# Performance work log

Measured on AMD Instinct MI355X. Metric: run time of the kernel, lower is better.

The kernel has to match this reference:

```python
import jax, jax.numpy as jnp
import numpy as np

L, T, D, H, NC = 4, 2, 128, 8, 7
DH = D // H
DFF = 4 * D
EPS = 1e-5


def _ln(x, w, b):
    m = jnp.mean(x, axis=-1, keepdims=True)
    v = jnp.mean((x - m) ** 2, axis=-1, keepdims=True)
    return (x - m) / jnp.sqrt(v + EPS) * w + b


def setup_inputs() -> dict:
    key = jax.random.key(0)
    ks = jax.random.split(key, 16)
    s = 0.02
    inp = {
        "x": jax.random.normal(ks[0], (65536, 1, 2 * D), dtype=jnp.float32),
        "token_proj_w": jax.random.normal(ks[1], (T * D, T * D), dtype=jnp.float32) * s,
        "token_proj_b": jnp.zeros((T * D,), jnp.float32),
        "pos_emb": jax.random.normal(ks[2], (1, T, D), dtype=jnp.float32),
        "qkv_w": jax.random.normal(ks[3], (L, 3 * D, D), dtype=jnp.float32) * s,
        "qkv_b": jnp.zeros((L, 3 * D), jnp.float32),
        "out_w": jax.random.normal(ks[4], (L, D, D), dtype=jnp.float32) * s,
        "out_b": jnp.zeros((L, D), jnp.float32),
        "ln1_w": jnp.ones((L, D), jnp.float32),
        "ln1_b": jnp.zeros((L, D), jnp.float32),
        "ff1_w": jax.random.normal(ks[5], (L, DFF, D), dtype=jnp.float32) * s,
        "ff1_b": jnp.zeros((L, DFF), jnp.float32),
        "ff2_w": jax.random.normal(ks[6], (L, D, DFF), dtype=jnp.float32) * s,
        "ff2_b": jnp.zeros((L, D), jnp.float32),
        "ln2_w": jnp.ones((L, D), jnp.float32),
        "ln2_b": jnp.zeros((L, D), jnp.float32),
        "lnf_w": jnp.ones((D,), jnp.float32),
        "lnf_b": jnp.zeros((D,), jnp.float32),
        "cls_ln_w": jnp.ones((D,), jnp.float32),
        "cls_ln_b": jnp.zeros((D,), jnp.float32),
        "cls_w": jax.random.normal(ks[7], (NC, D), dtype=jnp.float32) * s,
        "cls_b": jnp.zeros((NC,), jnp.float32),
    }
    return inp


def _forward(x, token_proj_w, token_proj_b, pos_emb, qkv_w, qkv_b, out_w, out_b,
             ln1_w, ln1_b, ff1_w, ff1_b, ff2_w, ff2_b, ln2_w, ln2_b,
             lnf_w, lnf_b, cls_ln_w, cls_ln_b, cls_w, cls_b):
    x = jnp.squeeze(x, 1)                                  # [B, 256]
    B = x.shape[0]
    tok = x @ token_proj_w.T + token_proj_b                # [B, 256]
    tok = tok.reshape(B, T, D) + pos_emb                   # [B, 2, 128]
    scale = 1.0 / jnp.sqrt(jnp.float32(DH))
    for i in range(L):
        # --- self-attention (post-norm, as in nn.TransformerEncoderLayer) ---
        qkv = jnp.einsum('btd,ed->bte', tok, qkv_w[i]) + qkv_b[i]   # [B,T,3D]
        q, k, v = jnp.split(qkv, 3, axis=-1)
        q = q.reshape(B, T, H, DH)
        k = k.reshape(B, T, H, DH)
        v = v.reshape(B, T, H, DH)
        scores = jnp.einsum('bqhd,bkhd->bhqk', q, k) * scale
        attn = jax.nn.softmax(scores, axis=-1)
        o = jnp.einsum('bhqk,bkhd->bqhd', attn, v).reshape(B, T, D)
        o = jnp.einsum('btd,ed->bte', o, out_w[i]) + out_b[i]
        tok = _ln(tok + o, ln1_w[i], ln1_b[i])
        # --- FFN ---
        h = jnp.einsum('btd,fd->btf', tok, ff1_w[i]) + ff1_b[i]
        h = jax.nn.gelu(h, approximate=False)
        h = jnp.einsum('btf,df->btd', h, ff2_w[i]) + ff2_b[i]
        tok = _ln(tok + h, ln2_w[i], ln2_b[i])
    tok = _ln(tok, lnf_w, lnf_b)                           # final encoder norm
    pooled = jnp.mean(tok, axis=1)                         # [B, D]
    out = _ln(pooled, cls_ln_w, cls_ln_b)
    out = jax.nn.gelu(out, approximate=False)
    return out @ cls_w.T + cls_b                           # [B, 7]


def reference(x, token_proj_w, token_proj_b, pos_emb, qkv_w, qkv_b, out_w, out_b,
              ln1_w, ln1_b, ff1_w, ff1_b, ff2_w, ff2_b, ln2_w, ln2_b,
              lnf_w, lnf_b, cls_ln_w, cls_ln_b, cls_w, cls_b):
    return _forward(x, token_proj_w, token_proj_b, pos_emb, qkv_w, qkv_b, out_w, out_b,
                    ln1_w, ln1_b, ff1_w, ff1_b, ff2_w, ff2_b, ln2_w, ln2_b,
                    lnf_w, lnf_b, cls_ln_w, cls_ln_b, cls_w, cls_b)
```

## Files before the change

### kernel.cpp

```cpp
#include <hip/hip_runtime.h>


#define DEV static __device__ __forceinline__

typedef __attribute__((ext_vector_type(8))) short short8;
typedef __attribute__((ext_vector_type(4))) float f32x4;

#define BS    32
#define MROWS 64
#define PITCH 136
#define LEPS  1e-5f

#define OFF_TPW  0
#define OFF_QKVW 65536
#define OFF_OUTW 262144
#define OFF_FF1W 327680
#define OFF_FF2W 589824
#define WS_ELEMS 851968

DEV unsigned short f2b(float f) {
  unsigned u = __float_as_uint(f);
  return (unsigned short)((u + 0x7fffu + ((u >> 16) & 1u)) >> 16);
}
DEV float b2f(unsigned short s) { return __uint_as_float((unsigned)s << 16); }

DEV f32x4 MFMA(short8 a, short8 b, f32x4 c) {
  return __builtin_amdgcn_mfma_f32_16x16x32_bf16(a, b, c, 0, 0, 0);
}

DEV float gelu_f(float x) {
  float u = 0.7978845608028654f * (x + 0.044715f * x * x * x);
  float e = __expf(2.0f * u);
  float t = 1.0f - 2.0f / (e + 1.0f);
  return 0.5f * x * (1.0f + t);
}

DEV short8 ldfrag(const unsigned short* tile, int rowBase, int kk, int lane) {
  return *(const short8*)(tile + (rowBase + (lane & 15)) * PITCH + kk * 32 + (lane >> 4) * 8);
}

DEV void stage_f32(unsigned short* dst, const float* __restrict__ src,
                   int srcPitch, int rows, int tid) {
  int total = rows * 8;
  for (int idx = tid; idx < total; idx += 256) {
    int r = idx >> 3, s = idx & 7;
    const float4* p = (const float4*)(src + (size_t)r * srcPitch + s * 16);
    float4 f0 = p[0], f1 = p[1], f2 = p[2], f3 = p[3];
    short8 lo, hi;
    lo[0] = (short)f2b(f0.x); lo[1] = (short)f2b(f0.y);
    lo[2] = (short)f2b(f0.z); lo[3] = (short)f2b(f0.w);
    lo[4] = (short)f2b(f1.x); lo[5] = (short)f2b(f1.y);
    lo[6] = (short)f2b(f1.z); lo[7] = (short)f2b(f1.w);
    hi[0] = (short)f2b(f2.x); hi[1] = (short)f2b(f2.y);
    hi[2] = (short)f2b(f2.z); hi[3] = (short)f2b(f2.w);
    hi[4] = (short)f2b(f3.x); hi[5] = (short)f2b(f3.y);
    hi[6] = (short)f2b(f3.z); hi[7] = (short)f2b(f3.w);
    *(short8*)(dst + r * PITCH + s * 16)     = lo;
    *(short8*)(dst + r * PITCH + s * 16 + 8) = hi;
  }
}

DEV void stage_w64(unsigned short* dst, const unsigned short* __restrict__ src,
                   int srcPitch, int tid) {
  for (int idx = tid; idx < 512; idx += 256) {
    int r = idx >> 3, s = idx & 7;
    const uint4* p = (const uint4*)(src + (size_t)r * srcPitch + s * 16);
    uint4 a = p[0], b = p[1];
    *(uint4*)(dst + r * PITCH + s * 16)     = a;
    *(uint4*)(dst + r * PITCH + s * 16 + 8) = b;
  }
}

DEV void ln_residual_write(f32x4 (&val)[2][4], const float* __restrict__ w,
                           const float* __restrict__ b, unsigned short* sTok,
                           float* sRedP, float* sRedF, int tid) {
  const int wave = tid >> 6, lane = tid & 63, g = lane >> 4, j = lane & 15;
  float ps[4][4], pq[4][4];
#pragma unroll
  for (int rt = 0; rt < 4; ++rt)
#pragma unroll
    for (int r = 0; r < 4; ++r) {
      float v0 = val[0][rt][r], v1 = val[1][rt][r];
      float s = v0 + v1, q = v0 * v0 + v1 * v1;
#pragma unroll
      for (int m = 1; m < 16; m <<= 1) {
        s += __shfl_xor(s, m, 16);
        q += __shfl_xor(q, m, 16);
      }
      ps[rt][r] = s; pq[rt][r] = q;
    }
  if (j == 0) {
#pragma unroll
    for (int rt = 0; rt < 4; ++rt)
#pragma unroll
      for (int r = 0; r < 4; ++r) {
        int row = rt * 16 + g * 4 + r;
        sRedP[row * 8 + wave * 2]     = ps[rt][r];
        sRedP[row * 8 + wave * 2 + 1] = pq[rt][r];
      }
  }
  __syncthreads();
  if (tid < 64) {
    float s = 0.f, q = 0.f;
#pragma unroll
    for (int wv = 0; wv < 4; ++wv) {
      s += sRedP[tid * 8 + wv * 2];
      q += sRedP[tid * 8 + wv * 2 + 1];
    }
    float mean = s * (1.f / 128.f);
    sRedF[tid * 2]     = mean;
    sRedF[tid * 2 + 1] = rsqrtf(q * (1.f / 128.f) - mean * mean + LEPS);
  }
  __syncthreads();
#pragma unroll
  for (int h = 0; h < 2; ++h) {
    int n = (h * 4 + wave) * 16 + j;
    float wn = w[n], bn = b[n];
#pragma unroll
    for (int rt = 0; rt < 4; ++rt)
#pragma unroll
      for (int r = 0; r < 4; ++r) {
        int row = rt * 16 + g * 4 + r;
        float mean = sRedF[row * 2], rstd = sRedF[row * 2 + 1];
        sTok[row * PITCH + n] = f2b((val[h][rt][r] - mean) * rstd * wn + bn);
      }
  }
  __syncthreads();
}

__global__ __launch_bounds__(256)
void prep_w(const float* __restrict__ tpw, const float* __restrict__ qkvw,
            const float* __restrict__ outw, const float* __restrict__ ff1w,
            const float* __restrict__ ff2w, unsigned short* __restrict__ wsb) {
  int i = blockIdx.x * 256 + threadIdx.x;
  if (i >= WS_ELEMS) return;
  float v;
  if (i < OFF_QKVW)      v = tpw[i - OFF_TPW];
  else if (i < OFF_OUTW) v = qkvw[i - OFF_QKVW];
  else if (i < OFF_FF1W) v = outw[i - OFF_OUTW];
  else if (i < OFF_FF2W) v = ff1w[i - OFF_FF1W];
  else                   v = ff2w[i - OFF_FF2W];
  wsb[i] = f2b(v);
}

#define STAGE_W(srcexpr, pitch)                         \
  do {                                                  \
    __syncthreads();                                    \
    stage_w64(sB, (srcexpr), (pitch), tid);             \
    __syncthreads();                                    \
  } while (0)

__global__ __launch_bounds__(256, 2)
void tx_fused(const float* __restrict__ x, const unsigned short* __restrict__ wsb,
              const float* __restrict__ tpb, const float* __restrict__ pos,
              const float* __restrict__ qkvb, const float* __restrict__ outb,
              const float* __restrict__ ln1w, const float* __restrict__ ln1b,
              const float* __restrict__ ff1b, const float* __restrict__ ff2b,
              const float* __restrict__ ln2w, const float* __restrict__ ln2b,
              const float* __restrict__ lnfw, const float* __restrict__ lnfb,
              const float* __restrict__ clnw, const float* __restrict__ clnb,
              const float* __restrict__ cw, const float* __restrict__ cb,
              float* __restrict__ out) {
  __shared__ unsigned short sTok[MROWS * PITCH];
  __shared__ unsigned short sStage[MROWS * PITCH];
  __shared__ unsigned short sB[64 * PITCH];
  __shared__ float sRedP[MROWS * 8];
  __shared__ float sRedF[MROWS * 2];

  const int tid  = threadIdx.x;
  const int wave = tid >> 6;
  const int lane = tid & 63;
  const int g = lane >> 4, j = lane & 15;
  const size_t s0 = (size_t)blockIdx.x * BS;

  const unsigned short* tpwB  = wsb + OFF_TPW;
  const unsigned short* qkvwB = wsb + OFF_QKVW;
  const unsigned short* outwB = wsb + OFF_OUTW;
  const unsigned short* ff1wB = wsb + OFF_FF1W;
  const unsigned short* ff2wB = wsb + OFF_FF2W;

  const f32x4 zero4 = {0.f, 0.f, 0.f, 0.f};

  f32x4 accTP[2][2][2];
#pragma unroll
  for (int nc = 0; nc < 2; ++nc)
#pragma unroll
    for (int h = 0; h < 2; ++h)
#pragma unroll
      for (int rt = 0; rt < 2; ++rt) accTP[nc][h][rt] = zero4;

  for (int kc = 0; kc < 2; ++kc) {
    __syncthreads();
    stage_f32(sStage, x + s0 * 256 + kc * 128, 256, BS, tid);
    for (int nc = 0; nc < 2; ++nc)
      for (int h = 0; h < 2; ++h) {
        STAGE_W(tpwB + (size_t)(nc * 128 + h * 64) * 256 + kc * 128, 256);
        short8 bf[4];
#pragma unroll
        for (int kk = 0; kk < 4; ++kk) bf[kk] = ldfrag(sB, wave * 16, kk, lane);
#pragma unroll
        for (int rt = 0; rt < 2; ++rt)
#pragma unroll
          for (int kk = 0; kk < 4; ++kk)
            accTP[nc][h][rt] = MFMA(ldfrag(sStage, rt * 16, kk, lane), bf[kk], accTP[nc][h][rt]);
      }
  }
  __syncthreads();
#pragma unroll
  for (int nc = 0; nc < 2; ++nc)
#pragma unroll
    for (int h = 0; h < 2; ++h) {
      int d = (h * 4 + wave) * 16 + j;
      float bias = tpb[nc * 128 + d] + pos[nc * 128 + d];
#pragma unroll
      for (int rt = 0; rt < 2; ++rt)
#pragma unroll
        for (int r = 0; r < 4; ++r) {
          int sm = rt * 16 + g * 4 + r;
          sTok[(2 * sm + nc) * PITCH + d] = f2b(accTP[nc][h][rt][r] + bias);
        }
    }
  __syncthreads();

  for (int li = 0; li < 4; ++li) {
    short8 aT[4][4];
#pragma unroll
    for (int rt = 0; rt < 4; ++rt)
#pragma unroll
      for (int kk = 0; kk < 4; ++kk) aT[rt][kk] = ldfrag(sTok, rt * 16, kk, lane);

    f32x4 acc[6][4];
#pragma unroll
    for (int a = 0; a < 6; ++a)
#pragma unroll
      for (int rt = 0; rt < 4; ++rt) acc[a][rt] = zero4;

    for (int nc = 0; nc < 3; ++nc)
      for (int h = 0; h < 2; ++h) {
        STAGE_W(qkvwB + (size_t)li * 49152 + (size_t)(nc * 128 + h * 64) * 128, 128);
        short8 bf[4];
#pragma unroll
        for (int kk = 0; kk < 4; ++kk) bf[kk] = ldfrag(sB, wave * 16, kk, lane);
        int a = nc * 2 + h;
#pragma unroll
        for (int rt = 0; rt < 4; ++rt)
#pragma unroll
          for (int kk = 0; kk < 4; ++kk)
            acc[a][rt] = MFMA(aT[rt][kk], bf[kk], acc[a][rt]);
      }
#pragma unroll
    for (int a = 0; a < 6; ++a) {
      int nc = a >> 1, h = a & 1;
      float bv = qkvb[li * 384 + nc * 128 + (h * 4 + wave) * 16 + j];
#pragma unroll
      for (int rt = 0; rt < 4; ++rt) acc[a][rt] += bv;
    }

#pragma unroll
    for (int hh = 0; hh < 2; ++hh) {
      int head = hh * 4 + wave;
#pragma unroll
      for (int rt = 0; rt < 4; ++rt)
#pragma unroll
        for (int sp = 0; sp < 2; ++sp) {
          int r0 = sp * 2, r1 = r0 + 1;
          float q0 = acc[hh][rt][r0],     q1 = acc[hh][rt][r1];
          float k0 = acc[2 + hh][rt][r0], k1 = acc[2 + hh][rt][r1];
          float s00 = q0 * k0, s01 = q0 * k1, s10 = q1 * k0, s11 = q1 * k1;
#pragma unroll
          for (int m = 1; m < 16; m <<= 1) {
            s00 += __shfl_xor(s00, m, 16);
            s01 += __shfl_xor(s01, m, 16);
            s10 += __shfl_xor(s10, m, 16);
            s11 += __shfl_xor(s11, m, 16);
          }
          s00 *= 0.25f; s01 *= 0.25f; s10 *= 0.25f; s11 *= 0.25f;
          float m0 = fmaxf(s00, s01), m1 = fmaxf(s10, s11);
          float e00 = __expf(s00 - m0), e01 = __expf(s01 - m0);
          float e10 = __expf(s10 - m1), e11 = __expf(s11 - m1);
          float i0 = 1.f / (e00 + e01), i1 = 1.f / (e10 + e11);
          float v0 = acc[4 + hh][rt][r0], v1 = acc[4 + hh][rt][r1];
          float o0 = (e00 * v0 + e01 * v1) * i0;
          float o1 = (e10 * v0 + e11 * v1) * i1;
          int rowb = rt * 16 + g * 4 + r0;
          int col  = head * 16 + j;
          sStage[rowb * PITCH + col]       = f2b(o0);
          sStage[(rowb + 1) * PITCH + col] = f2b(o1);
        }
    }

    f32x4 accO[2][4];
#pragma unroll
    for (int h = 0; h < 2; ++h)
#pragma unroll
      for (int rt = 0; rt < 4; ++rt) accO[h][rt] = zero4;

    for (int h = 0; h < 2; ++h) {
      STAGE_W(outwB + (size_t)li * 16384 + (size_t)h * 64 * 128, 128);
      short8 bf[4];
#pragma unroll
      for (int kk = 0; kk < 4; ++kk) bf[kk] = ldfrag(sB, wave * 16, kk, lane);
#pragma unroll
      for (int rt = 0; rt < 4; ++rt)
#pragma unroll
        for (int kk = 0; kk < 4; ++kk)
          accO[h][rt] = MFMA(ldfrag(sStage, rt * 16, kk, lane), bf[kk], accO[h][rt]);
    }
#pragma unroll
    for (int h = 0; h < 2; ++h) {
      int n = (h * 4 + wave) * 16 + j;
      float ob = outb[li * 128 + n];
#pragma unroll
      for (int rt = 0; rt < 4; ++rt)
#pragma unroll
        for (int r = 0; r < 4; ++r) {
          int row = rt * 16 + g * 4 + r;
          accO[h][rt][r] += ob + b2f(sTok[row * PITCH + n]);
        }
    }
    ln_residual_write(accO, ln1w + li * 128, ln1b + li * 128, sTok, sRedP, sRedF, tid);

    short8 aF[4][4];
#pragma unroll
    for (int rt = 0; rt < 4; ++rt)
#pragma unroll
      for (int kk = 0; kk < 4; ++kk) aF[rt][kk] = ldfrag(sTok, rt * 16, kk, lane);

    f32x4 accF[2][4];
#pragma unroll
    for (int h = 0; h < 2; ++h)
#pragma unroll
      for (int rt = 0; rt < 4; ++rt) accF[h][rt] = zero4;

    for (int fc = 0; fc < 4; ++fc) {
      f32x4 hacc[2][4];
#pragma unroll
      for (int h = 0; h < 2; ++h)
#pragma unroll
        for (int rt = 0; rt < 4; ++rt) hacc[h][rt] = zero4;

      for (int h = 0; h < 2; ++h) {
        STAGE_W(ff1wB + (size_t)li * 65536 + (size_t)(fc * 128 + h * 64) * 128, 128);
        short8 bf[4];
#pragma unroll
        for (int kk = 0; kk < 4; ++kk) bf[kk] = ldfrag(sB, wave * 16, kk, lane);
#pragma unroll
        for (int rt = 0; rt < 4; ++rt)
#pragma unroll
          for (int kk = 0; kk < 4; ++kk)
            hacc[h][rt] = MFMA(aF[rt][kk], bf[kk], hacc[h][rt]);
      }
#pragma unroll
      for (int h = 0; h < 2; ++h) {
        int nl = (h * 4 + wave) * 16 + j;
        float bb = ff1b[li * 512 + fc * 128 + nl];
#pragma unroll
        for (int rt = 0; rt < 4; ++rt)
#pragma unroll
          for (int r = 0; r < 4; ++r) {
            float hv = gelu_f(hacc[h][rt][r] + bb);
            sStage[(rt * 16 + g * 4 + r) * PITCH + nl] = f2b(hv);
          }
      }
      short8 aH[4][4];
      for (int h = 0; h < 2; ++h) {
        STAGE_W(ff2wB + (size_t)li * 65536 + (size_t)h * 64 * 512 + fc * 128, 512);
        if (h == 0) {
#pragma unroll
          for (int rt = 0; rt < 4; ++rt)
#pragma unroll
            for (int kk = 0; kk < 4; ++kk) aH[rt][kk] = ldfrag(sStage, rt * 16, kk, lane);
        }
        short8 bf[4];
#pragma unroll
        for (int kk = 0; kk < 4; ++kk) bf[kk] = ldfrag(sB, wave * 16, kk, lane);
#pragma unroll
        for (int rt = 0; rt < 4; ++rt)
#pragma unroll
          for (int kk = 0; kk < 4; ++kk)
            accF[h][rt] = MFMA(aH[rt][kk], bf[kk], accF[h][rt]);
      }
    }
#pragma unroll
    for (int h = 0; h < 2; ++h) {
      int n = (h * 4 + wave) * 16 + j;
      float fb = ff2b[li * 128 + n];
#pragma unroll
      for (int rt = 0; rt < 4; ++rt)
#pragma unroll
        for (int r = 0; r < 4; ++r) {
          int row = rt * 16 + g * 4 + r;
          accF[h][rt][r] += fb + b2f(sTok[row * PITCH + n]);
        }
    }
    ln_residual_write(accF, ln2w + li * 128, ln2b + li * 128, sTok, sRedP, sRedF, tid);
  }

  {
    int row = tid >> 2, q4 = tid & 3;
    const unsigned short* rp = sTok + row * PITCH + q4 * 32;
    float vb[32];
    float s = 0.f, sq = 0.f;
#pragma unroll
    for (int t8 = 0; t8 < 4; ++t8) {
      short8 v = *(const short8*)(rp + t8 * 8);
#pragma unroll
      for (int e = 0; e < 8; ++e) {
        float f = b2f((unsigned short)v[e]);
        vb[t8 * 8 + e] = f; s += f; sq += f * f;
      }
    }
    s  += __shfl_xor(s, 1, 4);  s  += __shfl_xor(s, 2, 4);
    sq += __shfl_xor(sq, 1, 4); sq += __shfl_xor(sq, 2, 4);
    float mean = s * (1.f / 128.f);
    float rstd = rsqrtf(sq * (1.f / 128.f) - mean * mean + LEPS);
    unsigned short* wp = sTok + row * PITCH + q4 * 32;
#pragma unroll
    for (int c = 0; c < 32; ++c) {
      int col = q4 * 32 + c;
      wp[c] = f2b((vb[c] - mean) * rstd * lnfw[col] + lnfb[col]);
    }
  }
  __syncthreads();
  {
    int sIdx = tid >> 3, oct = tid & 7;
    float pv[16];
    float s = 0.f, sq = 0.f;
#pragma unroll
    for (int t8 = 0; t8 < 2; ++t8) {
      short8 va  = *(const short8*)(sTok + (2 * sIdx) * PITCH + oct * 16 + t8 * 8);
      short8 vb2 = *(const short8*)(sTok + (2 * sIdx + 1) * PITCH + oct * 16 + t8 * 8);
#pragma unroll
      for (int e = 0; e < 8; ++e) {
        float f = 0.5f * (b2f((unsigned short)va[e]) + b2f((unsigned short)vb2[e]));
        pv[t8 * 8 + e] = f; s += f; sq += f * f;
      }
    }
    s  += __shfl_xor(s, 1, 8);  s  += __shfl_xor(s, 2, 8);  s  += __shfl_xor(s, 4, 8);
    sq += __shfl_xor(sq, 1, 8); sq += __shfl_xor(sq, 2, 8); sq += __shfl_xor(sq, 4, 8);
    float mean = s * (1.f / 128.f);
    float rstd = rsqrtf(sq * (1.f / 128.f) - mean * mean + LEPS);
    float gv[16];
#pragma unroll
    for (int c = 0; c < 16; ++c) {
      int col = oct * 16 + c;
      gv[c] = gelu_f((pv[c] - mean) * rstd * clnw[col] + clnb[col]);
    }
#pragma unroll
    for (int cc = 0; cc < 7; ++cc) {
      float p = 0.f;
#pragma unroll
      for (int c = 0; c < 16; ++c) p += gv[c] * cw[cc * 128 + oct * 16 + c];
      p += __shfl_xor(p, 1, 8); p += __shfl_xor(p, 2, 8); p += __shfl_xor(p, 4, 8);
      if (oct == 0) out[(s0 + sIdx) * 7 + cc] = p + cb[cc];
    }
  }
}

extern "C" void kernel_launch(void* const* d_in, const int* in_sizes, int n_in,
                              void* d_out, int out_size, void* d_ws, size_t ws_size,
                              hipStream_t stream) {
  const float* x    = (const float*)d_in[0];
  const float* tpw  = (const float*)d_in[1];
  const float* tpb  = (const float*)d_in[2];
  const float* pos  = (const float*)d_in[3];
  const float* qkvw = (const float*)d_in[4];
  const float* qkvb = (const float*)d_in[5];
  const float* outw = (const float*)d_in[6];
  const float* outb = (const float*)d_in[7];
  const float* ln1w = (const float*)d_in[8];
  const float* ln1b = (const float*)d_in[9];
  const float* ff1w = (const float*)d_in[10];
  const float* ff1b = (const float*)d_in[11];
  const float* ff2w = (const float*)d_in[12];
  const float* ff2b = (const float*)d_in[13];
  const float* ln2w = (const float*)d_in[14];
  const float* ln2b = (const float*)d_in[15];
  const float* lnfw = (const float*)d_in[16];
  const float* lnfb = (const float*)d_in[17];
  const float* clnw = (const float*)d_in[18];
  const float* clnb = (const float*)d_in[19];
  const float* cw   = (const float*)d_in[20];
  const float* cb   = (const float*)d_in[21];
  unsigned short* wsb = (unsigned short*)d_ws;

  int B = in_sizes[0] / 256;

  hipLaunchKernelGGL(prep_w, dim3((WS_ELEMS + 255) / 256), dim3(256), 0, stream,
                     tpw, qkvw, outw, ff1w, ff2w, wsb);
  hipLaunchKernelGGL(tx_fused, dim3(B / BS), dim3(256), 0, stream,
                     x, wsb, tpb, pos, qkvb, outb, ln1w, ln1b, ff1b, ff2b,
                     ln2w, ln2b, lnfw, lnfb, clnw, clnb, cw, cb, (float*)d_out);
}
```

Before: 777.0 us.

## Double-buffer weight tiles with register prefetch across the fused transformer kernel

Replaces the synchronous stage-then-compute weight staging with a ping-pong LDS buffer. The next 64x128 weight tile is loaded into registers before the current tile's MFMAs and written to the other buffer afterwards, which leaves one barrier per tile instead of two and hides global load latency behind compute. The input x is staged once as a full 256-wide row, and the next stage's weight prefetch is threaded through layer boundaries. The extra LDS buffer and prefetch registers, along with dropping the min-2-blocks launch bound, may lower occupancy.

```diff
diff --git a/kernel.cpp b/kernel.cpp
--- a/kernel.cpp
+++ b/kernel.cpp
@@ -9,6 +9,8 @@
 #define BS    32
 #define MROWS 64
 #define PITCH 136
+#define XP    272
+#define BUFE  (64 * PITCH)
 #define LEPS  1e-5f
 
 #define OFF_TPW  0
@@ -38,36 +40,25 @@
 DEV short8 ldfrag(const unsigned short* tile, int rowBase, int kk, int lane) {
   return *(const short8*)(tile + (rowBase + (lane & 15)) * PITCH + kk * 32 + (lane >> 4) * 8);
 }
-
-DEV void stage_f32(unsigned short* dst, const float* __restrict__ src,
-                   int srcPitch, int rows, int tid) {
-  int total = rows * 8;
-  for (int idx = tid; idx < total; idx += 256) {
-    int r = idx >> 3, s = idx & 7;
-    const float4* p = (const float4*)(src + (size_t)r * srcPitch + s * 16);
-    float4 f0 = p[0], f1 = p[1], f2 = p[2], f3 = p[3];
-    short8 lo, hi;
-    lo[0] = (short)f2b(f0.x); lo[1] = (short)f2b(f0.y);
-    lo[2] = (short)f2b(f0.z); lo[3] = (short)f2b(f0.w);
-    lo[4] = (short)f2b(f1.x); lo[5] = (short)f2b(f1.y);
-    lo[6] = (short)f2b(f1.z); lo[7] = (short)f2b(f1.w);
-    hi[0] = (short)f2b(f2.x); hi[1] = (short)f2b(f2.y);
-    hi[2] = (short)f2b(f2.z); hi[3] = (short)f2b(f2.w);
-    hi[4] = (short)f2b(f3.x); hi[5] = (short)f2b(f3.y);
-    hi[6] = (short)f2b(f3.z); hi[7] = (short)f2b(f3.w);
-    *(short8*)(dst + r * PITCH + s * 16)     = lo;
-    *(short8*)(dst + r * PITCH + s * 16 + 8) = hi;
-  }
-}
-
-DEV void stage_w64(unsigned short* dst, const unsigned short* __restrict__ src,
+DEV short8 ldfragX(const unsigned short* tile, int rowBase, int koff, int lane) {
+  return *(const short8*)(tile + (rowBase + (lane & 15)) * XP + koff + (lane >> 4) * 8);
+}
+
+DEV void tile_load(uint4 (&R)[4], const unsigned short* __restrict__ src,
                    int srcPitch, int tid) {
-  for (int idx = tid; idx < 512; idx += 256) {
-    int r = idx >> 3, s = idx & 7;
-    const uint4* p = (const uint4*)(src + (size_t)r * srcPitch + s * 16);
-    uint4 a = p[0], b = p[1];
-    *(uint4*)(dst + r * PITCH + s * 16)     = a;
-    *(uint4*)(dst + r * PITCH + s * 16 + 8) = b;
+#pragma unroll
+  for (int ii = 0; ii < 4; ++ii) {
+    int q = ii * 256 + tid;
+    int n = q >> 4, m = q & 15;
+    R[ii] = *(const uint4*)(src + (size_t)n * srcPitch + m * 8);
+  }
+}
+DEV void tile_write(const uint4 (&R)[4], unsigned short* dstW, int tid) {
+#pragma unroll
+  for (int ii = 0; ii < 4; ++ii) {
+    int q = ii * 256 + tid;
+    int n = q >> 4, m = q & 15;
+    *(uint4*)(dstW + n * PITCH + m * 8) = R[ii];
   }
 }
 
@@ -143,14 +134,15 @@
   wsb[i] = f2b(v);
 }
 
-#define STAGE_W(srcexpr, pitch)                         \
-  do {                                                  \
-    __syncthreads();                                    \
-    stage_w64(sB, (srcexpr), (pitch), tid);             \
-    __syncthreads();                                    \
+#define LOADW(srcexpr, pitch) tile_load(R, (srcexpr), (pitch), tid)
+#define FLUSH()                                            \
+  do {                                                     \
+    tile_write(R, sW + (cur ^ 1) * BUFE, tid);             \
+    __syncthreads();                                       \
+    cur ^= 1;                                              \
   } while (0)
 
-__global__ __launch_bounds__(256, 2)
+__global__ __launch_bounds__(256)
 void tx_fused(const float* __restrict__ x, const unsigned short* __restrict__ wsb,
               const float* __restrict__ tpb, const float* __restrict__ pos,
               const float* __restrict__ qkvb, const float* __restrict__ outb,
@@ -161,9 +153,9 @@
               const float* __restrict__ clnw, const float* __restrict__ clnb,
               const float* __restrict__ cw, const float* __restrict__ cb,
               float* __restrict__ out) {
-  __shared__ unsigned short sTok[MROWS * PITCH];
-  __shared__ unsigned short sStage[MROWS * PITCH];
-  __shared__ unsigned short sB[64 * PITCH];
+  __shared__ __align__(16) unsigned short sTok[MROWS * PITCH];
+  __shared__ __align__(16) unsigned short sStage[MROWS * PITCH];
+  __shared__ __align__(16) unsigned short sW[2 * BUFE];
   __shared__ float sRedP[MROWS * 8];
   __shared__ float sRedF[MROWS * 2];
 
@@ -180,6 +172,32 @@
   const unsigned short* ff2wB = wsb + OFF_FF2W;
 
   const f32x4 zero4 = {0.f, 0.f, 0.f, 0.f};
+  int cur = 0;
+  uint4 R[4];
+
+  LOADW(tpwB, 256);
+  {
+#pragma unroll
+    for (int it = 0; it < 2; ++it) {
+      int idx = it * 256 + tid;
+      int r = idx >> 4, s = idx & 15;
+      const float4* p = (const float4*)(x + (s0 + r) * 256 + s * 16);
+      float4 f0 = p[0], f1 = p[1], f2 = p[2], f3 = p[3];
+      short8 lo, hi;
+      lo[0] = (short)f2b(f0.x); lo[1] = (short)f2b(f0.y);
+      lo[2] = (short)f2b(f0.z); lo[3] = (short)f2b(f0.w);
+      lo[4] = (short)f2b(f1.x); lo[5] = (short)f2b(f1.y);
+      lo[6] = (short)f2b(f1.z); lo[7] = (short)f2b(f1.w);
+      hi[0] = (short)f2b(f2.x); hi[1] = (short)f2b(f2.y);
+      hi[2] = (short)f2b(f2.z); hi[3] = (short)f2b(f2.w);
+      hi[4] = (short)f2b(f3.x); hi[5] = (short)f2b(f3.y);
+      hi[6] = (short)f2b(f3.z); hi[7] = (short)f2b(f3.w);
+      *(short8*)(sStage + r * XP + s * 16)     = lo;
+      *(short8*)(sStage + r * XP + s * 16 + 8) = hi;
+    }
+  }
+  tile_write(R, sW, tid);
+  __syncthreads();
 
   f32x4 accTP[2][2][2];
 #pragma unroll
@@ -189,23 +207,28 @@
 #pragma unroll
       for (int rt = 0; rt < 2; ++rt) accTP[nc][h][rt] = zero4;
 
-  for (int kc = 0; kc < 2; ++kc) {
-    __syncthreads();
-    stage_f32(sStage, x + s0 * 256 + kc * 128, 256, BS, tid);
-    for (int nc = 0; nc < 2; ++nc)
-      for (int h = 0; h < 2; ++h) {
-        STAGE_W(tpwB + (size_t)(nc * 128 + h * 64) * 256 + kc * 128, 256);
-        short8 bf[4];
-#pragma unroll
-        for (int kk = 0; kk < 4; ++kk) bf[kk] = ldfrag(sB, wave * 16, kk, lane);
-#pragma unroll
-        for (int rt = 0; rt < 2; ++rt)
-#pragma unroll
-          for (int kk = 0; kk < 4; ++kk)
-            accTP[nc][h][rt] = MFMA(ldfrag(sStage, rt * 16, kk, lane), bf[kk], accTP[nc][h][rt]);
-      }
-  }
-  __syncthreads();
+#pragma unroll
+  for (int t = 0; t < 8; ++t) {
+    int kc = t >> 2, nc = (t >> 1) & 1, h = t & 1;
+    if (t < 7) {
+      int t2 = t + 1;
+      int kc2 = t2 >> 2, nc2 = (t2 >> 1) & 1, h2 = t2 & 1;
+      LOADW(tpwB + (size_t)(nc2 * 128 + h2 * 64) * 256 + kc2 * 128, 256);
+    } else {
+      LOADW(qkvwB, 128);
+    }
+    const unsigned short* bp = sW + cur * BUFE;
+    short8 bf[4];
+#pragma unroll
+    for (int kk = 0; kk < 4; ++kk) bf[kk] = ldfrag(bp, wave * 16, kk, lane);
+#pragma unroll
+    for (int rt = 0; rt < 2; ++rt)
+#pragma unroll
+      for (int kk = 0; kk < 4; ++kk)
+        accTP[nc][h][rt] = MFMA(ldfragX(sStage, rt * 16, kc * 128 + kk * 32, lane),
+                                bf[kk], accTP[nc][h][rt]);
+    FLUSH();
+  }
 #pragma unroll
   for (int nc = 0; nc < 2; ++nc)
 #pragma unroll
@@ -223,6 +246,11 @@
   __syncthreads();
 
   for (int li = 0; li < 4; ++li) {
+    const unsigned short* qkvL = qkvwB + (size_t)li * 49152;
+    const unsigned short* outL = outwB + (size_t)li * 16384;
+    const unsigned short* ff1L = ff1wB + (size_t)li * 65536;
+    const unsigned short* ff2L = ff2wB + (size_t)li * 65536;
+
     short8 aT[4][4];
 #pragma unroll
     for (int rt = 0; rt < 4; ++rt)
@@ -235,88 +263,110 @@
 #pragma unroll
       for (int rt = 0; rt < 4; ++rt) acc[a][rt] = zero4;
 
-    for (int nc = 0; nc < 3; ++nc)
+#pragma unroll
+    for (int t = 0; t < 6; ++t) {
+      LOADW(t < 5 ? qkvL + (size_t)(t + 1) * 8192 : outL, 128);
+      const unsigned short* bp = sW + cur * BUFE;
+      short8 bf[4];
+#pragma unroll
+      for (int kk = 0; kk < 4; ++kk) bf[kk] = ldfrag(bp, wave * 16, kk, lane);
+#pragma unroll
+      for (int rt = 0; rt < 4; ++rt)
+#pragma unroll
+        for (int kk = 0; kk < 4; ++kk)
+          acc[t][rt] = MFMA(aT[rt][kk], bf[kk], acc[t][rt]);
+      if (t == 5) {
+#pragma unroll
+        for (int a = 0; a < 6; ++a) {
+          int nc = a >> 1, h = a & 1;
+          float bv = qkvb[li * 384 + nc * 128 + (h * 4 + wave) * 16 + j];
+#pragma unroll
+          for (int rt = 0; rt < 4; ++rt) acc[a][rt] += bv;
+        }
+#pragma unroll
+        for (int hh = 0; hh < 2; ++hh) {
+          int head = hh * 4 + wave;
+#pragma unroll
+          for (int rt = 0; rt < 4; ++rt)
+#pragma unroll
+            for (int sp = 0; sp < 2; ++sp) {
+              int r0 = sp * 2, r1 = r0 + 1;
+              float q0 = acc[hh][rt][r0],     q1 = acc[hh][rt][r1];
+              float k0 = acc[2 + hh][rt][r0], k1 = acc[2 + hh][rt][r1];
+              float s00 = q0 * k0, s01 = q0 * k1, s10 = q1 * k0, s11 = q1 * k1;
+#pragma unroll
+              for (int m = 1; m < 16; m <<= 1) {
+                s00 += __shfl_xor(s00, m, 16);
+                s01 += __shfl_xor(s01, m, 16);
+                s10 += __shfl_xor(s10, m, 16);
+                s11 += __shfl_xor(s11, m, 16);
+              }
+              s00 *= 0.25f; s01 *= 0.25f; s10 *= 0.25f; s11 *= 0.25f;
+              float m0 = fmaxf(s00, s01), m1 = fmaxf(s10, s11);
+              float e00 = __expf(s00 - m0), e01 = __expf(s01 - m0);
+              float e10 = __expf(s10 - m1), e11 = __expf(s11 - m1);
+              float i0 = 1.f / (e00 + e01), i1 = 1.f / (e10 + e11);
+              float v0 = acc[4 + hh][rt][r0], v1 = acc[4 + hh][rt][r1];
+              float o0 = (e00 * v0 + e01 * v1) * i0;
+              float o1 = (e10 * v0 + e11 * v1) * i1;
+              int rowb = rt * 16 + g * 4 + r0;
+              int col  = head * 16 + j;
+              sStage[rowb * PITCH + col]       = f2b(o0);
+              sStage[(rowb + 1) * PITCH + col] = f2b(o1);
+            }
+        }
+      }
+      FLUSH();
+    }
+
+    f32x4 accO[2][4];
+#pragma unroll
+    for (int h = 0; h < 2; ++h)
+#pragma unroll
+      for (int rt = 0; rt < 4; ++rt) accO[h][rt] = zero4;
+
+    short8 aO[4][4];
+#pragma unroll
+    for (int rt = 0; rt < 4; ++rt)
+#pragma unroll
+      for (int kk = 0; kk < 4; ++kk) aO[rt][kk] = ldfrag(sStage, rt * 16, kk, lane);
+    {
+      LOADW(outL + 8192, 128);
+      const unsigned short* bp = sW + cur * BUFE;
+      short8 bf[4];
+#pragma unroll
+      for (int kk = 0; kk < 4; ++kk) bf[kk] = ldfrag(bp, wave * 16, kk, lane);
+#pragma unroll
+      for (int rt = 0; rt < 4; ++rt)
+#pragma unroll
+        for (int kk = 0; kk < 4; ++kk)
+          accO[0][rt] = MFMA(aO[rt][kk], bf[kk], accO[0][rt]);
+      FLUSH();
+    }
+    {
+      LOADW(ff1L, 128);
+      const unsigned short* bp = sW + cur * BUFE;
+      short8 bf[4];
+#pragma unroll
+      for (int kk = 0; kk < 4; ++kk) bf[kk] = ldfrag(bp, wave * 16, kk, lane);
+#pragma unroll
+      for (int rt = 0; rt < 4; ++rt)
+#pragma unroll
+        for (int kk = 0; kk < 4; ++kk)
+          accO[1][rt] = MFMA(aO[rt][kk], bf[kk], accO[1][rt]);
+#pragma unroll
       for (int h = 0; h < 2; ++h) {
-        STAGE_W(qkvwB + (size_t)li * 49152 + (size_t)(nc * 128 + h * 64) * 128, 128);
-        short8 bf[4];
-#pragma unroll
-        for (int kk = 0; kk < 4; ++kk) bf[kk] = ldfrag(sB, wave * 16, kk, lane);
-        int a = nc * 2 + h;
+        int n = (h * 4 + wave) * 16 + j;
+        float ob = outb[li * 128 + n];
 #pragma unroll
         for (int rt = 0; rt < 4; ++rt)
 #pragma unroll
-          for (int kk = 0; kk < 4; ++kk)
-            acc[a][rt] = MFMA(aT[rt][kk], bf[kk], acc[a][rt]);
-      }
-#pragma unroll
-    for (int a = 0; a < 6; ++a) {
-      int nc = a >> 1, h = a & 1;
-      float bv = qkvb[li * 384 + nc * 128 + (h * 4 + wave) * 16 + j];
-#pragma unroll
-      for (int rt = 0; rt < 4; ++rt) acc[a][rt] += bv;
-    }
-
-#pragma unroll
-    for (int hh = 0; hh < 2; ++hh) {
-      int head = hh * 4 + wave;
-#pragma unroll
-      for (int rt = 0; rt < 4; ++rt)
-#pragma unroll
-        for (int sp = 0; sp < 2; ++sp) {
-          int r0 = sp * 2, r1 = r0 + 1;
-          float q0 = acc[hh][rt][r0],     q1 = acc[hh][rt][r1];
-          float k0 = acc[2 + hh][rt][r0], k1 = acc[2 + hh][rt][r1];
-          float s00 = q0 * k0, s01 = q0 * k1, s10 = q1 * k0, s11 = q1 * k1;
-#pragma unroll
-          for (int m = 1; m < 16; m <<= 1) {
-            s00 += __shfl_xor(s00, m, 16);
-            s01 += __shfl_xor(s01, m, 16);
-            s10 += __shfl_xor(s10, m, 16);
-            s11 += __shfl_xor(s11, m, 16);
+          for (int r = 0; r < 4; ++r) {
+            int row = rt * 16 + g * 4 + r;
+            accO[h][rt][r] += ob + b2f(sTok[row * PITCH + n]);
           }
-          s00 *= 0.25f; s01 *= 0.25f; s10 *= 0.25f; s11 *= 0.25f;
-          float m0 = fmaxf(s00, s01), m1 = fmaxf(s10, s11);
-          float e00 = __expf(s00 - m0), e01 = __expf(s01 - m0);
-          float e10 = __expf(s10 - m1), e11 = __expf(s11 - m1);
-          float i0 = 1.f / (e00 + e01), i1 = 1.f / (e10 + e11);
-          float v0 = acc[4 + hh][rt][r0], v1 = acc[4 + hh][rt][r1];
-          float o0 = (e00 * v0 + e01 * v1) * i0;
-          float o1 = (e10 * v0 + e11 * v1) * i1;
-          int rowb = rt * 16 + g * 4 + r0;
-          int col  = head * 16 + j;
-          sStage[rowb * PITCH + col]       = f2b(o0);
-          sStage[(rowb + 1) * PITCH + col] = f2b(o1);
-        }
-    }
-
-    f32x4 accO[2][4];
-#pragma unroll
-    for (int h = 0; h < 2; ++h)
-#pragma unroll
-      for (int rt = 0; rt < 4; ++rt) accO[h][rt] = zero4;
-
-    for (int h = 0; h < 2; ++h) {
-      STAGE_W(outwB + (size_t)li * 16384 + (size_t)h * 64 * 128, 128);
-      short8 bf[4];
-#pragma unroll
-      for (int kk = 0; kk < 4; ++kk) bf[kk] = ldfrag(sB, wave * 16, kk, lane);
-#pragma unroll
-      for (int rt = 0; rt < 4; ++rt)
-#pragma unroll
-        for (int kk = 0; kk < 4; ++kk)
-          accO[h][rt] = MFMA(ldfrag(sStage, rt * 16, kk, lane), bf[kk], accO[h][rt]);
-    }
-#pragma unroll
-    for (int h = 0; h < 2; ++h) {
-      int n = (h * 4 + wave) * 16 + j;
-      float ob = outb[li * 128 + n];
-#pragma unroll
-      for (int rt = 0; rt < 4; ++rt)
-#pragma unroll
-        for (int r = 0; r < 4; ++r) {
-          int row = rt * 16 + g * 4 + r;
-          accO[h][rt][r] += ob + b2f(sTok[row * PITCH + n]);
-        }
+      }
+      FLUSH();
     }
     ln_residual_write(accO, ln1w + li * 128, ln1b + li * 128, sTok, sRedP, sRedF, tid);
 
@@ -338,47 +388,78 @@
       for (int h = 0; h < 2; ++h)
 #pragma unroll
         for (int rt = 0; rt < 4; ++rt) hacc[h][rt] = zero4;
-
-      for (int h = 0; h < 2; ++h) {
-        STAGE_W(ff1wB + (size_t)li * 65536 + (size_t)(fc * 128 + h * 64) * 128, 128);
+      {
+        LOADW(ff1L + (size_t)fc * 16384 + 8192, 128);
+        const unsigned short* bp = sW + cur * BUFE;
         short8 bf[4];
 #pragma unroll
-        for (int kk = 0; kk < 4; ++kk) bf[kk] = ldfrag(sB, wave * 16, kk, lane);
+        for (int kk = 0; kk < 4; ++kk) bf[kk] = ldfrag(bp, wave * 16, kk, lane);
 #pragma unroll
         for (int rt = 0; rt < 4; ++rt)
 #pragma unroll
           for (int kk = 0; kk < 4; ++kk)
-            hacc[h][rt] = MFMA(aF[rt][kk], bf[kk], hacc[h][rt]);
-      }
-#pragma unroll
-      for (int h = 0; h < 2; ++h) {
-        int nl = (h * 4 + wave) * 16 + j;
-        float bb = ff1b[li * 512 + fc * 128 + nl];
+            hacc[0][rt] = MFMA(aF[rt][kk], bf[kk], hacc[0][rt]);
+        FLUSH();
+      }
+      {
+        LOADW(ff2L + (size_t)fc * 128, 512);
+        const unsigned short* bp = sW + cur * BUFE;
+        short8 bf[4];
+#pragma unroll
+        for (int kk = 0; kk < 4; ++kk) bf[kk] = ldfrag(bp, wave * 16, kk, lane);
 #pragma unroll
         for (int rt = 0; rt < 4; ++rt)
 #pragma unroll
-          for (int r = 0; r < 4; ++r) {
-            float hv = gelu_f(hacc[h][rt][r] + bb);
-            sStage[(rt * 16 + g * 4 + r) * PITCH + nl] = f2b(hv);
-          }
+          for (int kk = 0; kk < 4; ++kk)
+            hacc[1][rt] = MFMA(aF[rt][kk], bf[kk], hacc[1][rt]);
+#pragma unroll
+        for (int h = 0; h < 2; ++h) {
+          int nl = (h * 4 + wave) * 16 + j;
+          float bb = ff1b[li * 512 + fc * 128 + nl];
+#pragma unroll
+          for (int rt = 0; rt < 4; ++rt)
+#pragma unroll
+            for (int r = 0; r < 4; ++r) {
+              float hv = gelu_f(hacc[h][rt][r] + bb);
+              sStage[(rt * 16 + g * 4 + r) * PITCH + nl] = f2b(hv);
+            }
+        }
+        FLUSH();
       }
       short8 aH[4][4];
-      for (int h = 0; h < 2; ++h) {
-        STAGE_W(ff2wB + (size_t)li * 65536 + (size_t)h * 64 * 512 + fc * 128, 512);
-        if (h == 0) {
-#pragma unroll
-          for (int rt = 0; rt < 4; ++rt)
-#pragma unroll
-            for (int kk = 0; kk < 4; ++kk) aH[rt][kk] = ldfrag(sStage, rt * 16, kk, lane);
-        }
+#pragma unroll
+      for (int rt = 0; rt < 4; ++rt)
+#pragma unroll
+        for (int kk = 0; kk < 4; ++kk) aH[rt][kk] = ldfrag(sStage, rt * 16, kk, lane);
+      {
+        LOADW(ff2L + (size_t)64 * 512 + fc * 128, 512);
+        const unsigned short* bp = sW + cur * BUFE;
         short8 bf[4];
 #pragma unroll
-        for (int kk = 0; kk < 4; ++kk) bf[kk] = ldfrag(sB, wave * 16, kk, lane);
+        for (int kk = 0; kk < 4; ++kk) bf[kk] = ldfrag(bp, wave * 16, kk, lane);
 #pragma unroll
         for (int rt = 0; rt < 4; ++rt)
 #pragma unroll
           for (int kk = 0; kk < 4; ++kk)
-            accF[h][rt] = MFMA(aH[rt][kk], bf[kk], accF[h][rt]);
+            accF[0][rt] = MFMA(aH[rt][kk], bf[kk], accF[0][rt]);
+        FLUSH();
+      }
+      {
+        bool hasNext = (fc < 3) || (li < 3);
+        if (fc < 3)      LOADW(ff1L + (size_t)(fc + 1) * 16384, 128);
+        else if (li < 3) LOADW(qkvL + 49152, 128);
+        const unsigned short* bp = sW + cur * BUFE;
+        short8 bf[4];
+#pragma unroll
+        for (int kk = 0; kk < 4; ++kk) bf[kk] = ldfrag(bp, wave * 16, kk, lane);
+#pragma unroll
+        for (int rt = 0; rt < 4; ++rt)
+#pragma unroll
+          for (int kk = 0; kk < 4; ++kk)
+            accF[1][rt] = MFMA(aH[rt][kk], bf[kk], accF[1][rt]);
+        if (hasNext) tile_write(R, sW + (cur ^ 1) * BUFE, tid);
+        __syncthreads();
+        cur ^= 1;
       }
     }
 #pragma unroll
@@ -460,6 +541,7 @@
 extern "C" void kernel_launch(void* const* d_in, const int* in_sizes, int n_in,
                               void* d_out, int out_size, void* d_ws, size_t ws_size,
                               hipStream_t stream) {
+  (void)n_in; (void)out_size; (void)ws_size;
   const float* x    = (const float*)d_in[0];
   const float* tpw  = (const float*)d_in[1];
   const float* tpb  = (const float*)d_in[2];
```

Result: slower. 1.264 ms (+62.7%).

## Load weight MFMA fragments directly from global memory instead of LDS staging

Applied to the files above, without the earlier changes.

Removes the shared-memory weight staging buffer and its two barriers per 64-column chunk. Each wave now reads its B-operand fragments straight from the global bf16 weight workspace, relying on L2/L1 caching. The input x is staged once as a full 256-wide bf16 tile rather than in two k-chunks. This cuts the barrier count and LDS traffic and frees LDS, in exchange for uncoalesced-ish global loads whose latency is exposed with no explicit prefetch.

```diff
diff --git a/kernel.cpp b/kernel.cpp
--- a/kernel.cpp
+++ b/kernel.cpp
@@ -9,6 +9,7 @@
 #define BS    32
 #define MROWS 64
 #define PITCH 136
+#define XP    272
 #define LEPS  1e-5f
 
 #define OFF_TPW  0
@@ -38,37 +39,13 @@
 DEV short8 ldfrag(const unsigned short* tile, int rowBase, int kk, int lane) {
   return *(const short8*)(tile + (rowBase + (lane & 15)) * PITCH + kk * 32 + (lane >> 4) * 8);
 }
-
-DEV void stage_f32(unsigned short* dst, const float* __restrict__ src,
-                   int srcPitch, int rows, int tid) {
-  int total = rows * 8;
-  for (int idx = tid; idx < total; idx += 256) {
-    int r = idx >> 3, s = idx & 7;
-    const float4* p = (const float4*)(src + (size_t)r * srcPitch + s * 16);
-    float4 f0 = p[0], f1 = p[1], f2 = p[2], f3 = p[3];
-    short8 lo, hi;
-    lo[0] = (short)f2b(f0.x); lo[1] = (short)f2b(f0.y);
-    lo[2] = (short)f2b(f0.z); lo[3] = (short)f2b(f0.w);
-    lo[4] = (short)f2b(f1.x); lo[5] = (short)f2b(f1.y);
-    lo[6] = (short)f2b(f1.z); lo[7] = (short)f2b(f1.w);
-    hi[0] = (short)f2b(f2.x); hi[1] = (short)f2b(f2.y);
-    hi[2] = (short)f2b(f2.z); hi[3] = (short)f2b(f2.w);
-    hi[4] = (short)f2b(f3.x); hi[5] = (short)f2b(f3.y);
-    hi[6] = (short)f2b(f3.z); hi[7] = (short)f2b(f3.w);
-    *(short8*)(dst + r * PITCH + s * 16)     = lo;
-    *(short8*)(dst + r * PITCH + s * 16 + 8) = hi;
-  }
-}
-
-DEV void stage_w64(unsigned short* dst, const unsigned short* __restrict__ src,
-                   int srcPitch, int tid) {
-  for (int idx = tid; idx < 512; idx += 256) {
-    int r = idx >> 3, s = idx & 7;
-    const uint4* p = (const uint4*)(src + (size_t)r * srcPitch + s * 16);
-    uint4 a = p[0], b = p[1];
-    *(uint4*)(dst + r * PITCH + s * 16)     = a;
-    *(uint4*)(dst + r * PITCH + s * 16 + 8) = b;
-  }
+DEV short8 ldfragX(const unsigned short* tile, int rowBase, int koff, int lane) {
+  return *(const short8*)(tile + (rowBase + (lane & 15)) * XP + koff + (lane >> 4) * 8);
+}
+DEV short8 ldBg(const unsigned short* __restrict__ base, int pitch, int colBase,
+                int koff, int kk, int lane) {
+  return *(const short8*)(base + (size_t)(colBase + (lane & 15)) * pitch +
+                          koff + kk * 32 + (lane >> 4) * 8);
 }
 
 DEV void ln_residual_write(f32x4 (&val)[2][4], const float* __restrict__ w,
@@ -143,13 +120,6 @@
   wsb[i] = f2b(v);
 }
 
-#define STAGE_W(srcexpr, pitch)                         \
-  do {                                                  \
-    __syncthreads();                                    \
-    stage_w64(sB, (srcexpr), (pitch), tid);             \
-    __syncthreads();                                    \
-  } while (0)
-
 __global__ __launch_bounds__(256, 2)
 void tx_fused(const float* __restrict__ x, const unsigned short* __restrict__ wsb,
               const float* __restrict__ tpb, const float* __restrict__ pos,
@@ -161,9 +131,8 @@
               const float* __restrict__ clnw, const float* __restrict__ clnb,
               const float* __restrict__ cw, const float* __restrict__ cb,
               float* __restrict__ out) {
-  __shared__ unsigned short sTok[MROWS * PITCH];
-  __shared__ unsigned short sStage[MROWS * PITCH];
-  __shared__ unsigned short sB[64 * PITCH];
+  __shared__ __align__(16) unsigned short sTok[MROWS * PITCH];
+  __shared__ __align__(16) unsigned short sStage[MROWS * PITCH];
   __shared__ float sRedP[MROWS * 8];
   __shared__ float sRedF[MROWS * 2];
 
@@ -181,6 +150,28 @@
 
   const f32x4 zero4 = {0.f, 0.f, 0.f, 0.f};
 
+  {
+#pragma unroll
+    for (int it = 0; it < 2; ++it) {
+      int idx = it * 256 + tid;
+      int r = idx >> 4, s = idx & 15;
+      const float4* p = (const float4*)(x + (s0 + r) * 256 + s * 16);
+      float4 f0 = p[0], f1 = p[1], f2 = p[2], f3 = p[3];
+      short8 lo, hi;
+      lo[0] = (short)f2b(f0.x); lo[1] = (short)f2b(f0.y);
+      lo[2] = (short)f2b(f0.z); lo[3] = (short)f2b(f0.w);
+      lo[4] = (short)f2b(f1.x); lo[5] = (short)f2b(f1.y);
+      lo[6] = (short)f2b(f1.z); lo[7] = (short)f2b(f1.w);
+      hi[0] = (short)f2b(f2.x); hi[1] = (short)f2b(f2.y);
+      hi[2] = (short)f2b(f2.z); hi[3] = (short)f2b(f2.w);
+      hi[4] = (short)f2b(f3.x); hi[5] = (short)f2b(f3.y);
+      hi[6] = (short)f2b(f3.z); hi[7] = (short)f2b(f3.w);
+      *(short8*)(sStage + r * XP + s * 16)     = lo;
+      *(short8*)(sStage + r * XP + s * 16 + 8) = hi;
+    }
+  }
+  __syncthreads();
+
   f32x4 accTP[2][2][2];
 #pragma unroll
   for (int nc = 0; nc < 2; ++nc)
@@ -189,22 +180,24 @@
 #pragma unroll
       for (int rt = 0; rt < 2; ++rt) accTP[nc][h][rt] = zero4;
 
-  for (int kc = 0; kc < 2; ++kc) {
-    __syncthreads();
-    stage_f32(sStage, x + s0 * 256 + kc * 128, 256, BS, tid);
+#pragma unroll
+  for (int kc = 0; kc < 2; ++kc)
+#pragma unroll
     for (int nc = 0; nc < 2; ++nc)
+#pragma unroll
       for (int h = 0; h < 2; ++h) {
-        STAGE_W(tpwB + (size_t)(nc * 128 + h * 64) * 256 + kc * 128, 256);
+        int cb = nc * 128 + (h * 4 + wave) * 16;
         short8 bf[4];
 #pragma unroll
-        for (int kk = 0; kk < 4; ++kk) bf[kk] = ldfrag(sB, wave * 16, kk, lane);
+        for (int kk = 0; kk < 4; ++kk)
+          bf[kk] = ldBg(tpwB, 256, cb, kc * 128, kk, lane);
 #pragma unroll
         for (int rt = 0; rt < 2; ++rt)
 #pragma unroll
           for (int kk = 0; kk < 4; ++kk)
-            accTP[nc][h][rt] = MFMA(ldfrag(sStage, rt * 16, kk, lane), bf[kk], accTP[nc][h][rt]);
-      }
-  }
+            accTP[nc][h][rt] = MFMA(ldfragX(sStage, rt * 16, kc * 128 + kk * 32, lane),
+                                    bf[kk], accTP[nc][h][rt]);
+      }
   __syncthreads();
 #pragma unroll
   for (int nc = 0; nc < 2; ++nc)
@@ -223,6 +216,11 @@
   __syncthreads();
 
   for (int li = 0; li < 4; ++li) {
+    const unsigned short* qkvL = qkvwB + (size_t)li * 49152;
+    const unsigned short* outL = outwB + (size_t)li * 16384;
+    const unsigned short* ff1L = ff1wB + (size_t)li * 65536;
+    const unsigned short* ff2L = ff2wB + (size_t)li * 65536;
+
     short8 aT[4][4];
 #pragma unroll
     for (int rt = 0; rt < 4; ++rt)
@@ -235,12 +233,14 @@
 #pragma unroll
       for (int rt = 0; rt < 4; ++rt) acc[a][rt] = zero4;
 
+#pragma unroll
     for (int nc = 0; nc < 3; ++nc)
+#pragma unroll
       for (int h = 0; h < 2; ++h) {
-        STAGE_W(qkvwB + (size_t)li * 49152 + (size_t)(nc * 128 + h * 64) * 128, 128);
+        int cb = nc * 128 + (h * 4 + wave) * 16;
         short8 bf[4];
 #pragma unroll
-        for (int kk = 0; kk < 4; ++kk) bf[kk] = ldfrag(sB, wave * 16, kk, lane);
+        for (int kk = 0; kk < 4; ++kk) bf[kk] = ldBg(qkvL, 128, cb, 0, kk, lane);
         int a = nc * 2 + h;
 #pragma unroll
         for (int rt = 0; rt < 4; ++rt)
@@ -288,23 +288,30 @@
           sStage[(rowb + 1) * PITCH + col] = f2b(o1);
         }
     }
+    __syncthreads();
+
+    short8 aO[4][4];
+#pragma unroll
+    for (int rt = 0; rt < 4; ++rt)
+#pragma unroll
+      for (int kk = 0; kk < 4; ++kk) aO[rt][kk] = ldfrag(sStage, rt * 16, kk, lane);
 
     f32x4 accO[2][4];
 #pragma unroll
     for (int h = 0; h < 2; ++h)
 #pragma unroll
       for (int rt = 0; rt < 4; ++rt) accO[h][rt] = zero4;
-
+#pragma unroll
     for (int h = 0; h < 2; ++h) {
-      STAGE_W(outwB + (size_t)li * 16384 + (size_t)h * 64 * 128, 128);
+      int cb = (h * 4 + wave) * 16;
       short8 bf[4];
 #pragma unroll
-      for (int kk = 0; kk < 4; ++kk) bf[kk] = ldfrag(sB, wave * 16, kk, lane);
+      for (int kk = 0; kk < 4; ++kk) bf[kk] = ldBg(outL, 128, cb, 0, kk, lane);
 #pragma unroll
       for (int rt = 0; rt < 4; ++rt)
 #pragma unroll
         for (int kk = 0; kk < 4; ++kk)
-          accO[h][rt] = MFMA(ldfrag(sStage, rt * 16, kk, lane), bf[kk], accO[h][rt]);
+          accO[h][rt] = MFMA(aO[rt][kk], bf[kk], accO[h][rt]);
     }
 #pragma unroll
     for (int h = 0; h < 2; ++h) {
@@ -338,18 +345,19 @@
       for (int h = 0; h < 2; ++h)
 #pragma unroll
         for (int rt = 0; rt < 4; ++rt) hacc[h][rt] = zero4;
-
+#pragma unroll
       for (int h = 0; h < 2; ++h) {
-        STAGE_W(ff1wB + (size_t)li * 65536 + (size_t)(fc * 128 + h * 64) * 128, 128);
+        int cb = fc * 128 + (h * 4 + wave) * 16;
         short8 bf[4];
 #pragma unroll
-        for (int kk = 0; kk < 4; ++kk) bf[kk] = ldfrag(sB, wave * 16, kk, lane);
+        for (int kk = 0; kk < 4; ++kk) bf[kk] = ldBg(ff1L, 128, cb, 0, kk, lane);
 #pragma unroll
         for (int rt = 0; rt < 4; ++rt)
 #pragma unroll
           for (int kk = 0; kk < 4; ++kk)
             hacc[h][rt] = MFMA(aF[rt][kk], bf[kk], hacc[h][rt]);
       }
+      __syncthreads();
 #pragma unroll
       for (int h = 0; h < 2; ++h) {
         int nl = (h * 4 + wave) * 16 + j;
@@ -362,18 +370,19 @@
             sStage[(rt * 16 + g * 4 + r) * PITCH + nl] = f2b(hv);
           }
       }
+      __syncthreads();
       short8 aH[4][4];
+#pragma unroll
+      for (int rt = 0; rt < 4; ++rt)
+#pragma unroll
+        for (int kk = 0; kk < 4; ++kk) aH[rt][kk] = ldfrag(sStage, rt * 16, kk, lane);
+#pragma unroll
       for (int h = 0; h < 2; ++h) {
-        STAGE_W(ff2wB + (size_t)li * 65536 + (size_t)h * 64 * 512 + fc * 128, 512);
-        if (h == 0) {
-#pragma unroll
-          for (int rt = 0; rt < 4; ++rt)
-#pragma unroll
-            for (int kk = 0; kk < 4; ++kk) aH[rt][kk] = ldfrag(sStage, rt * 16, kk, lane);
-        }
+        int cb = (h * 4 + wave) * 16;
         short8 bf[4];
 #pragma unroll
-        for (int kk = 0; kk < 4; ++kk) bf[kk] = ldfrag(sB, wave * 16, kk, lane);
+        for (int kk = 0; kk < 4; ++kk)
+          bf[kk] = ldBg(ff2L, 512, cb, fc * 128, kk, lane);
 #pragma unroll
         for (int rt = 0; rt < 4; ++rt)
 #pragma unroll
@@ -460,6 +469,7 @@
 extern "C" void kernel_launch(void* const* d_in, const int* in_sizes, int n_in,
                               void* d_out, int out_size, void* d_ws, size_t ws_size,
                               hipStream_t stream) {
+  (void)n_in; (void)out_size; (void)ws_size;
   const float* x    = (const float*)d_in[0];
   const float* tpw  = (const float*)d_in[1];
   const float* tpb  = (const float*)d_in[2];
```

Result: faster. 719.3 us, median of 2 (-7.4%).
